# Optimization experiments

Hardware: AMD Instinct MI355X
Metric: run time of the kernel (lower is better)

## Reference

```python
import jax, jax.numpy as jnp
import numpy as np

N_BITS = 16
BATCH = 4194304  # 2**22 tokens
TABLE_SIZE = 2 ** (N_BITS - 1)  # largest CUMULATIVE/FLIP context is n_bits-1 bits


def setup_inputs() -> dict:
    key = jax.random.key(0)
    k1, k2 = jax.random.split(key)
    # input bit tensor [batch, n_bits], values in {0,1}; index n_bits-1 is bit 0 (LSB)
    bits = jax.random.randint(k1, (BATCH, N_BITS), 0, 2, dtype=jnp.int32)
    # per-bit-position RAM lookup tables, padded to the max address space.
    # Binary contents {0,1}, stored as float32 so the flip/XOR math is expressible.
    tables = (jax.random.uniform(k2, (N_BITS, TABLE_SIZE)) < 0.5).astype(jnp.float32)
    return {"bits": bits, "tables": tables}


def reference(bits, tables):
    """BitLevelMapper forward, CUMULATIVE context + FLIP output mode.

    bits:   [B, n_bits] int32 in {0,1}, array index n_bits-1-k holds bit value k (LSB=k=0)
    tables: [n_bits, 2^(n_bits-1)] float32 in {0,1}; row i is the RAM/LUT for bit_pos i.
    For bit_pos i the context is the lowest i bits (bit0..bit_{i-1});
    address = sum_k context_bit_k * 2^k; flip = table[i, address];
    output bit i = input bit i XOR flip.
    """
    n_bits = bits.shape[1]
    bits_rev = bits[:, ::-1]                      # [B, n] column k = bit value k
    k = jnp.arange(n_bits)
    # W[i, k] = 2^k if k < i else 0  -> addr_i = sum_{k<i} bit_k * 2^k (addr_0 = 0)
    W = jnp.where(k[None, :] < k[:, None], (1 << k)[None, :], 0).astype(jnp.int32)
    addr = bits_rev @ W.T                          # [B, n] int32 RAM addresses per bit_pos
    flip = tables[k[None, :], addr]                # [B, n] gather: tables[i, addr[b, i]]
    x = bits_rev.astype(tables.dtype)
    out_rev = x + flip - 2.0 * x * flip            # XOR expressed arithmetically
    return out_rev[:, ::-1]                        # back to original bit-array layout
```

## Files before the change

kernel.cpp:

```cpp
#include <hip/hip_runtime.h>
#include <hip/hip_bf16.h>


#define PACK_WORDS 2048

typedef float vfloat4 __attribute__((ext_vector_type(4)));

__global__ __launch_bounds__(256) void
pack_tables_kernel(const float* __restrict__ tables, unsigned* __restrict__ packed) {
    int g = blockIdx.x * blockDim.x + threadIdx.x;
    bool val = false;
    if (g < 65535) {
        int i = 31 - __clz(g + 1);
        int a = g - ((1 << i) - 1);
        val = tables[i * 32768 + a] != 0.0f;
    }
    unsigned long long m = __ballot(val);
    if ((threadIdx.x & 63) == 0) {
        packed[(g >> 5)]     = (unsigned)m;
        packed[(g >> 5) + 1] = (unsigned)(m >> 32);
    }
}

__global__ __launch_bounds__(256) void
compress_kernel(const int4* __restrict__ bits4, unsigned short* __restrict__ rowv) {
    int t = blockIdx.x * 256 + threadIdx.x;
    int4 m = bits4[t];
    unsigned nb = (unsigned)((m.x << 3) | (m.y << 2) | (m.z << 1) | m.w);
    unsigned part = nb << (12 - ((t & 3) << 2));
    part |= (unsigned)__shfl_xor((int)part, 1, 64);
    part |= (unsigned)__shfl_xor((int)part, 2, 64);
    if ((t & 3) == 0)
        rowv[t >> 2] = (unsigned short)part;
}

__global__ __launch_bounds__(256) void
expand_kernel(const unsigned short* __restrict__ rowv,
              const unsigned* __restrict__ packed,
              vfloat4* __restrict__ out4) {
    __shared__ unsigned tab[PACK_WORDS];
    {
        const int4* p4 = (const int4*)packed;
        int4* t4 = (int4*)tab;
        t4[threadIdx.x]       = p4[threadIdx.x];
        t4[threadIdx.x + 256] = p4[threadIdx.x + 256];
    }
    __syncthreads();

    const size_t base = (size_t)blockIdx.x * 1024 + threadIdx.x;
    const int q4 = (int)(threadIdx.x & 3) << 2;
    #pragma unroll
    for (int it = 0; it < 4; ++it) {
        size_t t = base + (size_t)it * 256;
        unsigned v = rowv[t >> 2];
        float o[4];
        #pragma unroll
        for (int j = 0; j < 4; ++j) {
            int i = 15 - q4 - j;
            unsigned mask = (1u << i) - 1u;
            unsigned bidx = mask + (v & mask);
            unsigned fl   = tab[bidx >> 5] >> (bidx & 31u);
            o[j] = (float)(((v >> i) ^ fl) & 1u);
        }
        vfloat4 f = {o[0], o[1], o[2], o[3]};
        __builtin_nontemporal_store(f, &out4[t]);
    }
}

extern "C" void kernel_launch(void* const* d_in, const int* in_sizes, int n_in,
                              void* d_out, int out_size, void* d_ws, size_t ws_size,
                              hipStream_t stream) {
    const int*      bits   = (const int*)d_in[0];
    const float*    tables = (const float*)d_in[1];
    float*          out    = (float*)d_out;
    unsigned*       packed = (unsigned*)d_ws;
    unsigned short* rowv   = (unsigned short*)((char*)d_ws + 8192);

    int nrows    = in_sizes[0] / 16;
    int nquarter = nrows * 4;

    pack_tables_kernel<<<65536 / 256, 256, 0, stream>>>(tables, packed);

    compress_kernel<<<nquarter / 256, 256, 0, stream>>>((const int4*)bits, rowv);

    expand_kernel<<<nquarter / 1024, 256, 0, stream>>>(rowv, packed,
                                                       (vfloat4*)out);
}
```

Measured before the change: 429.9 us.

## Fuse bit compression into expand kernel, dropping intermediate row buffer

```diff
diff --git a/kernel.cpp b/kernel.cpp
--- a/kernel.cpp
+++ b/kernel.cpp
@@ -5,6 +5,7 @@
 #define PACK_WORDS 2048
 
 typedef float vfloat4 __attribute__((ext_vector_type(4)));
+typedef int   vint4   __attribute__((ext_vector_type(4)));
 
 __global__ __launch_bounds__(256) void
 pack_tables_kernel(const float* __restrict__ tables, unsigned* __restrict__ packed) {
@@ -23,36 +24,35 @@
 }
 
 __global__ __launch_bounds__(256) void
-compress_kernel(const int4* __restrict__ bits4, unsigned short* __restrict__ rowv) {
-    int t = blockIdx.x * 256 + threadIdx.x;
-    int4 m = bits4[t];
-    unsigned nb = (unsigned)((m.x << 3) | (m.y << 2) | (m.z << 1) | m.w);
-    unsigned part = nb << (12 - ((t & 3) << 2));
-    part |= (unsigned)__shfl_xor((int)part, 1, 64);
-    part |= (unsigned)__shfl_xor((int)part, 2, 64);
-    if ((t & 3) == 0)
-        rowv[t >> 2] = (unsigned short)part;
-}
-
-__global__ __launch_bounds__(256) void
-expand_kernel(const unsigned short* __restrict__ rowv,
-              const unsigned* __restrict__ packed,
-              vfloat4* __restrict__ out4) {
+fused_kernel(const vint4* __restrict__ bits4,
+             const unsigned* __restrict__ packed,
+             vfloat4* __restrict__ out4) {
     __shared__ unsigned tab[PACK_WORDS];
     {
-        const int4* p4 = (const int4*)packed;
-        int4* t4 = (int4*)tab;
+        const vint4* p4 = (const vint4*)packed;
+        vint4* t4 = (vint4*)tab;
         t4[threadIdx.x]       = p4[threadIdx.x];
         t4[threadIdx.x + 256] = p4[threadIdx.x + 256];
     }
+
+    const size_t base = (size_t)blockIdx.x * 1024 + threadIdx.x;
+
+    vint4 m[4];
+    #pragma unroll
+    for (int it = 0; it < 4; ++it)
+        m[it] = __builtin_nontemporal_load(&bits4[base + (size_t)it * 256]);
+
     __syncthreads();
 
-    const size_t base = (size_t)blockIdx.x * 1024 + threadIdx.x;
     const int q4 = (int)(threadIdx.x & 3) << 2;
     #pragma unroll
     for (int it = 0; it < 4; ++it) {
         size_t t = base + (size_t)it * 256;
-        unsigned v = rowv[t >> 2];
+        unsigned nb = (unsigned)((m[it][0] << 3) | (m[it][1] << 2) |
+                                 (m[it][2] << 1) |  m[it][3]);
+        unsigned v = nb << (12 - q4);
+        v |= (unsigned)__shfl_xor((int)v, 1, 64);
+        v |= (unsigned)__shfl_xor((int)v, 2, 64);
         float o[4];
         #pragma unroll
         for (int j = 0; j < 4; ++j) {
@@ -70,19 +70,16 @@
 extern "C" void kernel_launch(void* const* d_in, const int* in_sizes, int n_in,
                               void* d_out, int out_size, void* d_ws, size_t ws_size,
                               hipStream_t stream) {
-    const int*      bits   = (const int*)d_in[0];
-    const float*    tables = (const float*)d_in[1];
-    float*          out    = (float*)d_out;
-    unsigned*       packed = (unsigned*)d_ws;
-    unsigned short* rowv   = (unsigned short*)((char*)d_ws + 8192);
+    const int*   bits   = (const int*)d_in[0];
+    const float* tables = (const float*)d_in[1];
+    float*       out    = (float*)d_out;
+    unsigned*    packed = (unsigned*)d_ws;
 
     int nrows    = in_sizes[0] / 16;
     int nquarter = nrows * 4;
 
     pack_tables_kernel<<<65536 / 256, 256, 0, stream>>>(tables, packed);
 
-    compress_kernel<<<nquarter / 256, 256, 0, stream>>>((const int4*)bits, rowv);
-
-    expand_kernel<<<nquarter / 1024, 256, 0, stream>>>(rowv, packed,
-                                                       (vfloat4*)out);
+    fused_kernel<<<nquarter / 1024, 256, 0, stream>>>((const vint4*)bits, packed,
+                                                      (vfloat4*)out);
 }
```

New measurement: 416.8 us. -3.0%, faster.
